# Optimization experiments

Measured on AMD Instinct MI355X. Metric: run time of the kernel, lower is better.

## Reference

```python
import jax, jax.numpy as jnp
import numpy as np

B, Q, NCLS1, C = 8, 900, 11, 256
NUM_ANCHOR = 100
H, W = 200, 200


def _make_view(b):
    # maps homogeneous (x0, y0, x1, y1, 1) box coords (meters-ish) to BEV pixels:
    # pixel = 20 * coord + 100  (keeps random boxes inside the 200x200 grid)
    v = np.zeros((5, 5), dtype=np.float32)
    for i in range(4):
        v[i, i] = 20.0
        v[i, 4] = 100.0
    v[4, 4] = 1.0
    return jnp.asarray(np.broadcast_to(v, (b, 5, 5)).copy())


def setup_inputs() -> dict:
    key = jax.random.key(0)
    k1, k2, k3 = jax.random.split(key, 3)
    return {
        "pred_boxes": jax.random.normal(k1, (B, Q, 4), dtype=jnp.float32),
        "pred_logits": jax.random.normal(k2, (B, Q, NCLS1), dtype=jnp.float32),
        "box_feats": jax.random.normal(k3, (B, Q, C), dtype=jnp.float32),
        "view": _make_view(B),
    }


def _box_to_bev(pred_boxes, pred_logits, box_feats, view):
    # scores = max over non-background classes of softmax(logits)
    scores = jnp.max(jax.nn.softmax(pred_logits, axis=-1)[..., :-1], axis=-1)  # [b,Q]
    _, idx = jax.lax.top_k(scores, NUM_ANCHOR)                                 # [b,N]

    boxes = jnp.take_along_axis(pred_boxes, idx[:, :, None], axis=1)[..., :4]  # [b,N,4]
    feats = jnp.take_along_axis(box_feats, idx[:, :, None], axis=1)            # [b,N,C]

    cx, cy = boxes[..., 0], boxes[..., 1]
    w, h = jnp.exp(boxes[..., 2]), jnp.exp(boxes[..., 3])
    xyxy = jnp.stack([cx - 0.5 * w, cy - 0.5 * h, cx + 0.5 * w, cy + 0.5 * h], axis=-1)
    xyxy1 = jnp.concatenate([xyxy, jnp.ones_like(xyxy[..., :1])], axis=-1)     # [b,N,5]

    coords = jnp.einsum("bij,bnj->bni", view, xyxy1)[..., :4].astype(jnp.int32)
    x0 = jnp.clip(coords[..., 0], 0, W)
    y0 = jnp.clip(coords[..., 1], 0, H)
    x1 = jnp.clip(coords[..., 2], 0, W)
    y1 = jnp.clip(coords[..., 3], 0, H)

    ys = jnp.arange(H, dtype=jnp.int32)
    xs = jnp.arange(W, dtype=jnp.int32)
    row = (ys[None, None, :] >= y0[:, :, None]) & (ys[None, None, :] < y1[:, :, None])  # [b,N,H]
    col = (xs[None, None, :] >= x0[:, :, None]) & (xs[None, None, :] < x1[:, :, None])  # [b,N,W]
    region = row[:, :, :, None] & col[:, :, None, :]                                    # [b,N,H,W]

    bev = jnp.einsum("bnhw,bnc->bhwc", region.astype(feats.dtype), feats)  # [b,H,W,C]
    mask = jnp.any(region, axis=1)                                          # [b,H,W]
    return bev, mask


def reference(pred_boxes, pred_logits, box_feats, view):
    return _box_to_bev(pred_boxes, pred_logits, box_feats, view)
```

## Files before the change

kernel.cpp:

```cpp
#include <hip/hip_runtime.h>
#include <math.h>

#define B_    8
#define Q_    900
#define NCLS_ 11
#define NANC_ 100
#define H_    200
#define W_    200
#define C_    256
#define HHALF 100
#define CHNK_ 113

typedef float f32x4_ __attribute__((ext_vector_type(4)));

__global__ __launch_bounds__(128) void segdet_topk_kernel(
    const float* __restrict__ pred_boxes,
    const float* __restrict__ pred_logits,
    const float* __restrict__ view,
    int*  __restrict__ ws_idx,
    int4* __restrict__ ws_box)
{
    const int b     = blockIdx.x >> 3;
    const int chunk = blockIdx.x & 7;
    const int tid   = threadIdx.x;

    __shared__ __align__(16) float sc[Q_];

    for (int q2 = tid; q2 < Q_; q2 += 128) {
        const float* l = pred_logits + (b * Q_ + q2) * NCLS_;
        float v[NCLS_];
        float m = -INFINITY;
        #pragma unroll
        for (int i = 0; i < NCLS_; ++i) { v[i] = l[i]; m = fmaxf(m, v[i]); }
        float s = 0.0f, e10 = -INFINITY;
        #pragma unroll
        for (int i = 0; i < NCLS_; ++i) {
            float e = expf(v[i] - m);
            s += e;
            if (i < NCLS_ - 1) e10 = fmaxf(e10, e);
        }
        sc[q2] = e10 / s;
    }
    __syncthreads();

    const int q = chunk * CHNK_ + tid;
    if (tid < CHNK_ && q < Q_) {
        const float my = sc[q];
        int rank = 0;
        #pragma unroll 4
        for (int j4 = 0; j4 < Q_ / 4; ++j4) {
            const float4 o = *(const float4*)&sc[j4 * 4];
            const int j = j4 * 4;
            rank += (o.x > my) || (o.x == my && (j + 0) < q);
            rank += (o.y > my) || (o.y == my && (j + 1) < q);
            rank += (o.z > my) || (o.z == my && (j + 2) < q);
            rank += (o.w > my) || (o.w == my && (j + 3) < q);
        }
        if (rank < NANC_) {
            const float* bx = pred_boxes + (b * Q_ + q) * 4;
            double cx = (double)bx[0], cy = (double)bx[1];
            double w  = exp((double)bx[2]);
            double h  = exp((double)bx[3]);
            double p[5] = { cx - 0.5 * w, cy - 0.5 * h,
                            cx + 0.5 * w, cy + 0.5 * h, 1.0 };
            const float* v5 = view + b * 25;
            int ico[4];
            #pragma unroll
            for (int i = 0; i < 4; ++i) {
                double acc = 0.0;
                #pragma unroll
                for (int j = 0; j < 5; ++j) acc += (double)v5[i * 5 + j] * p[j];
                ico[i] = (int)acc;
            }
            int x0 = min(max(ico[0], 0), W_);
            int y0 = min(max(ico[1], 0), H_);
            int x1 = min(max(ico[2], 0), W_);
            int y1 = min(max(ico[3], 0), H_);
            const int slot = b * NANC_ + rank;
            ws_idx[slot] = q;
            ws_box[slot] = make_int4(x0, y0, x1, y1);
        }
    }
}

__device__ __forceinline__ void nt_store4(float* p, float4 v) {
    f32x4_ nv = { v.x, v.y, v.z, v.w };
    __builtin_nontemporal_store(nv, (f32x4_*)p);
}

__global__ __launch_bounds__(256) void segdet_bev_kernel(
    const float* __restrict__ box_feats,
    const int*   __restrict__ ws_idx,
    const int4*  __restrict__ ws_box,
    float* __restrict__ bev,
    float* __restrict__ mask)
{
    const int hidx = blockIdx.x / B_;
    const int b    = blockIdx.x % B_;
    const int h    = (hidx & 1) ? (HHALF - 1 - (hidx >> 1)) : (HHALF + (hidx >> 1));

    const int tid = threadIdx.x;
    const int ln  = tid & 63;
    const int wv  = tid >> 6;

    __shared__ int s_box[NANC_];
    __shared__ int s_nact;
    __shared__ int s_nopen[W_];
    __shared__ int s_ofs[W_ + 1];
    __shared__ int s_evpos[W_];
    __shared__ int s_ent[2 * NANC_];
    __shared__ int s_wsum[4];
    __shared__ int s_wtot[4];
    __shared__ int s_plow;

    if (tid < 64) {
        int na = 0;
        #pragma unroll
        for (int it = 0; it < 2; ++it) {
            int k = it * 64 + ln;
            bool act = false;
            int packed = 0;
            if (k < NANC_) {
                int4 bx = ws_box[b * NANC_ + k];
                int qi  = ws_idx[b * NANC_ + k];
                act = (bx.y <= h) && (h < bx.w) && (bx.x < bx.z);
                packed = bx.x | (bx.z << 8) | (qi << 16);
            }
            unsigned long long ball = __ballot(act);
            int pos = na + (int)__popcll(ball & ((1ull << ln) - 1ull));
            if (act) s_box[pos] = packed;
            na += (int)__popcll(ball);
        }
        if (ln == 0) s_nact = na;
    }
    __syncthreads();

    const int nact = s_nact;
    float* obase = bev + (size_t)(b * H_ + h) * W_ * C_ + ln * 4;
    float* mrow  = mask + (size_t)(b * H_ + h) * W_;

    if (nact == 0) {
        const float4 z = make_float4(0.f, 0.f, 0.f, 0.f);
        for (int w = wv; w < W_; w += 4)
            nt_store4(obase + (size_t)w * C_, z);
        if (tid < W_) __builtin_nontemporal_store(0.0f, &mrow[tid]);
        return;
    }

    int ntot = 0;
    if (tid < W_) {
        int nopen = 0, nclose = 0, cov = 0;
        for (int k = 0; k < nact; ++k) {
            int pk = s_box[k];
            int x0 = pk & 0xFF, x1 = (pk >> 8) & 0xFF;
            nopen  += (x0 == tid);
            nclose += (x1 == tid);
            cov    += (x0 <= tid) && (tid < x1);
        }
        s_nopen[tid] = nopen;
        ntot = nopen + nclose;
        __builtin_nontemporal_store((cov > 0) ? 1.0f : 0.0f, &mrow[tid]);
    }

    int incl = ntot;
    #pragma unroll
    for (int d = 1; d < 64; d <<= 1) {
        int u = __shfl_up(incl, d);
        incl = (ln >= d) ? incl + u : incl;
    }
    if (ln == 63) s_wsum[wv] = incl;

    const bool flag = (tid < W_) && (ntot > 0);
    const unsigned long long bal = __ballot(flag);
    if (ln == 0) s_wtot[wv] = (int)__popcll(bal);
    if (wv == 1 && ln == 0)
        s_plow = (int)__popcll(bal & ((1ull << 37) - 1ull));
    __syncthreads();

    int prev = 0;
    #pragma unroll
    for (int j = 0; j < 4; ++j) prev += (j < wv) ? s_wsum[j] : 0;
    const int ne = s_wsum[0] + s_wsum[1] + s_wsum[2] + s_wsum[3];
    if (tid < W_) s_ofs[tid] = prev + incl - ntot;
    if (tid == 0) s_ofs[W_] = ne;

    const int nev = s_wtot[0] + s_wtot[1] + s_wtot[2] + s_wtot[3];
    int eoff = 0;
    #pragma unroll
    for (int j = 0; j < 4; ++j) eoff += (j < wv) ? s_wtot[j] : 0;
    if (flag) s_evpos[eoff + (int)__popcll(bal & ((1ull << ln) - 1ull))] = tid;
    __syncthreads();

    if (tid < nact) {
        int pk = s_box[tid];
        int x0 = pk & 0xFF, x1 = (pk >> 8) & 0xFF, q = pk >> 16;
        int ro = 0, rc = 0;
        for (int j = 0; j < tid; ++j) {
            int pj = s_box[j];
            ro += ((pj & 0xFF) == x0);
            rc += (((pj >> 8) & 0xFF) == x1);
        }
        s_ent[s_ofs[x0] + ro] = q;
        if (x1 < W_) s_ent[s_ofs[x1] + s_nopen[x1] + rc] = q | (1 << 31);
    }
    __syncthreads();

    const bool upper = (wv >= 2);
    const int  wbeg  = upper ? (HHALF + (wv - 2)) : wv;
    const int  wlim  = upper ? W_ : HHALF;
    const int  p_lo  = s_wtot[0] + s_plow;

    const float* fbase = box_feats + (size_t)b * Q_ * C_ + ln * 4;

    float4 acc = make_float4(0.f, 0.f, 0.f, 0.f);
    int cnt = 0;
    if (upper) {
        for (int k = 0; k < nact; ++k) {
            int pk = s_box[k];
            int x0 = pk & 0xFF, x1 = (pk >> 8) & 0xFF;
            if (x0 <= HHALF && HHALF < x1) {
                const float4 f = *(const float4*)(fbase + (size_t)(pk >> 16) * C_);
                acc.x += f.x; acc.y += f.y; acc.z += f.z; acc.w += f.w;
                ++cnt;
            }
        }
    }
    int p = upper ? p_lo : 0;
    int nextpix = (p < nev) ? s_evpos[p] : W_;
    for (int w = wbeg; w < wlim; w += 2) {
        while (w >= nextpix) {
            int e1 = s_ofs[nextpix + 1];
            for (int e = s_ofs[nextpix]; e < e1; ++e) {
                int ent = s_ent[e];
                int q = ent & 0xFFFF;
                const float4 f = *(const float4*)(fbase + (size_t)q * C_);
                if (ent < 0) { acc.x -= f.x; acc.y -= f.y; acc.z -= f.z; acc.w -= f.w; --cnt; }
                else         { acc.x += f.x; acc.y += f.y; acc.z += f.z; acc.w += f.w; ++cnt; }
            }
            ++p;
            nextpix = (p < nev) ? s_evpos[p] : W_;
        }
        if (cnt == 0) acc = make_float4(0.f, 0.f, 0.f, 0.f);
        nt_store4(obase + (size_t)w * C_, acc);
    }
}

extern "C" void kernel_launch(void* const* d_in, const int* in_sizes, int n_in,
                              void* d_out, int out_size, void* d_ws, size_t ws_size,
                              hipStream_t stream) {
    const float* pred_boxes  = (const float*)d_in[0];
    const float* pred_logits = (const float*)d_in[1];
    const float* box_feats   = (const float*)d_in[2];
    const float* view        = (const float*)d_in[3];

    float* bev  = (float*)d_out;
    float* mask = bev + (size_t)B_ * H_ * W_ * C_;

    int*  ws_idx = (int*)d_ws;
    int4* ws_box = (int4*)((char*)d_ws + 3200);

    segdet_topk_kernel<<<B_ * 8, 128, 0, stream>>>(pred_boxes, pred_logits, view,
                                                   ws_idx, ws_box);
    segdet_bev_kernel<<<B_ * H_, 256, 0, stream>>>(box_feats, ws_idx, ws_box,
                                                   bev, mask);
}
```

Before: 103.1 us.

## Stage event feature rows into LDS with double-buffered async loads in BEV sweep

```diff
diff --git a/kernel.cpp b/kernel.cpp
--- a/kernel.cpp
+++ b/kernel.cpp
@@ -10,6 +10,7 @@
 #define C_    256
 #define HHALF 100
 #define CHNK_ 113
+#define CHEV_ 16
 
 typedef float f32x4_ __attribute__((ext_vector_type(4)));
 
@@ -83,9 +84,15 @@
     }
 }
 
-__device__ __forceinline__ void nt_store4(float* p, float4 v) {
-    f32x4_ nv = { v.x, v.y, v.z, v.w };
-    __builtin_nontemporal_store(nv, (f32x4_*)p);
+__device__ __forceinline__ void nt_store4(float* p, f32x4_ v) {
+    __builtin_nontemporal_store(v, (f32x4_*)p);
+}
+
+__device__ __forceinline__ void gload_lds_16(const float* g, float* l) {
+    __builtin_amdgcn_global_load_lds(
+        (const __attribute__((address_space(1))) void*)g,
+        (__attribute__((address_space(3))) void*)l,
+        16, 0, 0);
 }
 
 __global__ __launch_bounds__(256) void segdet_bev_kernel(
@@ -103,15 +110,13 @@
     const int ln  = tid & 63;
     const int wv  = tid >> 6;
 
+    __shared__ __align__(16) float s_chunk[2][CHEV_ * C_];
     __shared__ int s_box[NANC_];
     __shared__ int s_nact;
     __shared__ int s_nopen[W_];
     __shared__ int s_ofs[W_ + 1];
-    __shared__ int s_evpos[W_];
     __shared__ int s_ent[2 * NANC_];
     __shared__ int s_wsum[4];
-    __shared__ int s_wtot[4];
-    __shared__ int s_plow;
 
     if (tid < 64) {
         int na = 0;
@@ -140,7 +145,7 @@
     float* mrow  = mask + (size_t)(b * H_ + h) * W_;
 
     if (nact == 0) {
-        const float4 z = make_float4(0.f, 0.f, 0.f, 0.f);
+        const f32x4_ z = {0.f, 0.f, 0.f, 0.f};
         for (int w = wv; w < W_; w += 4)
             nt_store4(obase + (size_t)w * C_, z);
         if (tid < W_) __builtin_nontemporal_store(0.0f, &mrow[tid]);
@@ -169,12 +174,6 @@
         incl = (ln >= d) ? incl + u : incl;
     }
     if (ln == 63) s_wsum[wv] = incl;
-
-    const bool flag = (tid < W_) && (ntot > 0);
-    const unsigned long long bal = __ballot(flag);
-    if (ln == 0) s_wtot[wv] = (int)__popcll(bal);
-    if (wv == 1 && ln == 0)
-        s_plow = (int)__popcll(bal & ((1ull << 37) - 1ull));
     __syncthreads();
 
     int prev = 0;
@@ -183,12 +182,6 @@
     const int ne = s_wsum[0] + s_wsum[1] + s_wsum[2] + s_wsum[3];
     if (tid < W_) s_ofs[tid] = prev + incl - ntot;
     if (tid == 0) s_ofs[W_] = ne;
-
-    const int nev = s_wtot[0] + s_wtot[1] + s_wtot[2] + s_wtot[3];
-    int eoff = 0;
-    #pragma unroll
-    for (int j = 0; j < 4; ++j) eoff += (j < wv) ? s_wtot[j] : 0;
-    if (flag) s_evpos[eoff + (int)__popcll(bal & ((1ull << ln) - 1ull))] = tid;
     __syncthreads();
 
     if (tid < nact) {
@@ -200,49 +193,57 @@
             ro += ((pj & 0xFF) == x0);
             rc += (((pj >> 8) & 0xFF) == x1);
         }
-        s_ent[s_ofs[x0] + ro] = q;
-        if (x1 < W_) s_ent[s_ofs[x1] + s_nopen[x1] + rc] = q | (1 << 31);
-    }
-    __syncthreads();
-
-    const bool upper = (wv >= 2);
-    const int  wbeg  = upper ? (HHALF + (wv - 2)) : wv;
-    const int  wlim  = upper ? W_ : HHALF;
-    const int  p_lo  = s_wtot[0] + s_plow;
+        s_ent[s_ofs[x0] + ro] = q | (x0 << 10);
+        if (x1 < W_)
+            s_ent[s_ofs[x1] + s_nopen[x1] + rc] =
+                (int)((unsigned)q | ((unsigned)x1 << 10) | 0x80000000u);
+    }
+    __syncthreads();
 
     const float* fbase = box_feats + (size_t)b * Q_ * C_ + ln * 4;
-
-    float4 acc = make_float4(0.f, 0.f, 0.f, 0.f);
+    const int nchunk = (ne + CHEV_ - 1) / CHEV_;
+
+#define STAGE_(CI)                                                            \
+    {                                                                         \
+        const int base_ = (CI) * CHEV_;                                       \
+        float* dst_ = &s_chunk[(CI) & 1][0];                                  \
+        _Pragma("unroll")                                                     \
+        for (int j = 0; j < 4; ++j) {                                         \
+            const int e_ = base_ + wv * 4 + j;                                \
+            if (e_ < ne) {                                                    \
+                const int q_ = s_ent[e_] & 0x3FF;                             \
+                gload_lds_16(fbase + (size_t)q_ * C_,                         \
+                             dst_ + (wv * 4 + j) * C_);                       \
+            }                                                                 \
+        }                                                                     \
+    }
+
+    STAGE_(0);
+    __syncthreads();
+
+    f32x4_ acc = {0.f, 0.f, 0.f, 0.f};
     int cnt = 0;
-    if (upper) {
-        for (int k = 0; k < nact; ++k) {
-            int pk = s_box[k];
-            int x0 = pk & 0xFF, x1 = (pk >> 8) & 0xFF;
-            if (x0 <= HHALF && HHALF < x1) {
-                const float4 f = *(const float4*)(fbase + (size_t)(pk >> 16) * C_);
-                acc.x += f.x; acc.y += f.y; acc.z += f.z; acc.w += f.w;
-                ++cnt;
-            }
-        }
-    }
-    int p = upper ? p_lo : 0;
-    int nextpix = (p < nev) ? s_evpos[p] : W_;
-    for (int w = wbeg; w < wlim; w += 2) {
-        while (w >= nextpix) {
-            int e1 = s_ofs[nextpix + 1];
-            for (int e = s_ofs[nextpix]; e < e1; ++e) {
-                int ent = s_ent[e];
-                int q = ent & 0xFFFF;
-                const float4 f = *(const float4*)(fbase + (size_t)q * C_);
-                if (ent < 0) { acc.x -= f.x; acc.y -= f.y; acc.z -= f.z; acc.w -= f.w; --cnt; }
-                else         { acc.x += f.x; acc.y += f.y; acc.z += f.z; acc.w += f.w; ++cnt; }
-            }
-            ++p;
-            nextpix = (p < nev) ? s_evpos[p] : W_;
-        }
-        if (cnt == 0) acc = make_float4(0.f, 0.f, 0.f, 0.f);
+    int w = wv;
+    for (int ci = 0; ci < nchunk; ++ci) {
+        if (ci + 1 < nchunk) STAGE_(ci + 1);
+        const int ebeg = ci * CHEV_;
+        const int eend = (ne < ebeg + CHEV_) ? ne : (ebeg + CHEV_);
+        const float* cb = &s_chunk[ci & 1][0];
+        for (int e = ebeg; e < eend; ++e) {
+            const int ent = s_ent[e];
+            const int pe  = (ent >> 10) & 0xFF;
+            for (; w < pe; w += 4)
+                nt_store4(obase + (size_t)w * C_, acc);
+            const f32x4_ f = *(const f32x4_*)&cb[(e - ebeg) * C_ + ln * 4];
+            if (ent < 0) { acc -= f; --cnt; }
+            else         { acc += f; ++cnt; }
+            if (cnt == 0) acc = (f32x4_){0.f, 0.f, 0.f, 0.f};
+        }
+        __syncthreads();
+    }
+#undef STAGE_
+    for (; w < W_; w += 4)
         nt_store4(obase + (size_t)w * C_, acc);
-    }
 }
 
 extern "C" void kernel_launch(void* const* d_in, const int* in_sizes, int n_in,
```

Result: faster. 101.0 us (-2.0%).
